# Optimization experiments

Hardware: AMD Instinct MI355X
Metric: run time of the kernel (lower is better)

Reference implementation:

```python
import jax, jax.numpy as jnp
import numpy as np

EPSILON = 0.1      # entropic regularization
N_ITERS = 50       # Sinkhorn fixed-point iterations
EPS_STAB = 1e-6    # numerical stabilizer (max(eps_stab, 1e-6) in original)
N, M, D = 8192, 8192, 128


def _sinkhorn_cost(X, Y):
    # squared Euclidean cost matrix (n, m)
    x2 = jnp.sum(X * X, axis=-1)
    y2 = jnp.sum(Y * Y, axis=-1)
    C = jnp.maximum(x2[:, None] + y2[None, :] - 2.0 * (X @ Y.T), 0.0)
    K = jnp.exp(-C / EPSILON)
    n, m = X.shape[0], Y.shape[0]
    a = jnp.full((n,), 1.0 / n, dtype=C.dtype)
    b = jnp.full((m,), 1.0 / m, dtype=C.dtype)

    def step(uv, _):
        u, v = uv
        Kv = K @ v + EPS_STAB
        u = jnp.where(jnp.abs(Kv) < EPS_STAB, a, a / jnp.maximum(Kv, EPS_STAB))
        Ktu = K.T @ u + EPS_STAB
        v = jnp.where(jnp.abs(Ktu) < EPS_STAB, b, b / jnp.maximum(Ktu, EPS_STAB))
        return (u, v), None

    (u, v), _ = jax.lax.scan(step, (jnp.ones_like(a), jnp.ones_like(b)), None, length=N_ITERS)
    # cost = sum(pi * C) with pi = u[:,None] * K * v[None,:], fused via einsum
    return jnp.einsum('i,ij,ij,j->', u, K, C, v)


def setup_inputs() -> dict:
    key = jax.random.key(0)
    k1, k2 = jax.random.split(key)
    # scale so squared distances ~O(1), commensurate with EPSILON
    X = jax.random.normal(k1, (N, D), dtype=jnp.float32) * 0.05
    Y = jax.random.normal(k2, (M, D), dtype=jnp.float32) * 0.05
    return {"X": X, "Y": Y}


def reference(X, Y):
    ot_xy = _sinkhorn_cost(X, Y)
    ot_xx = _sinkhorn_cost(X, jax.lax.stop_gradient(X))
    ot_yy = _sinkhorn_cost(Y, jax.lax.stop_gradient(Y))
    div = ot_xy - 0.5 * (ot_xx + ot_yy)
    div = jnp.where(jnp.isfinite(div), div, jnp.zeros_like(div))
    return jnp.maximum(div, 0.0)
```

## Files before the change

### kernel.cpp

```cpp
#include <hip/hip_runtime.h>

#define NPTS 8192
#define DIM  128
#define WPREP(x) (0.015625f / ((x) + 1.28e-4f))

typedef short s16x8 __attribute__((ext_vector_type(8)));
typedef float f32x4 __attribute__((ext_vector_type(4)));
typedef float f32x2 __attribute__((ext_vector_type(2)));

__device__ __forceinline__ ushort f2bf(float f) {
  unsigned u = __float_as_uint(f);
  u += 0x7fffu + ((u >> 16) & 1u);
  return (ushort)(u >> 16);
}
__device__ __forceinline__ float bf2f(ushort b) {
  return __uint_as_float(((unsigned)b) << 16);
}

__device__ __forceinline__ unsigned char fp8_enc_sw(float f) {
  if (f < 0.015625f) {
    int mi = (int)rintf(f * 512.0f);
    return (unsigned char)(mi >= 8 ? 0x08 : mi);
  }
  unsigned u = __float_as_uint(f);
  unsigned r = u + 0xfffffu + ((u >> 20) & 1u);
  int e = (int)((r >> 23) & 0xff) - 127;
  unsigned mant = (r >> 20) & 7u;
  if (e > 8 || (e == 8 && mant > 6)) return 0x7e;
  return (unsigned char)(((e + 7) << 3) | mant);
}
__device__ __forceinline__ float fp8_dec_sw(unsigned b) {
  unsigned E = (b >> 3) & 15u, M = b & 7u;
  float n = __uint_as_float(((E + 120u) << 23) | (M << 20));
  float s = (float)M * 0.001953125f;
  return E ? n : s;
}
__device__ __forceinline__ unsigned char enc1(float f) {
#if __has_builtin(__builtin_amdgcn_cvt_pk_fp8_f32)
  return (unsigned char)(__builtin_amdgcn_cvt_pk_fp8_f32(f, f, 0, false) & 0xff);
#else
  return fp8_enc_sw(f);
#endif
}
template <bool HI>
__device__ __forceinline__ f32x2 dec2(unsigned w) {
#if __has_builtin(__builtin_amdgcn_cvt_pk_f32_fp8)
  return __builtin_amdgcn_cvt_pk_f32_fp8((int)w, HI);
#else
  f32x2 r;
  r.x = fp8_dec_sw(HI ? ((w >> 16) & 0xffu) : (w & 0xffu));
  r.y = fp8_dec_sw(HI ? (w >> 24) : ((w >> 8) & 0xffu));
  return r;
#endif
}

__device__ __forceinline__ int swz(int j) { return j + 2 * (j >> 5); }
#define WSZ (NPTS + 2 * (NPTS / 32) + 8)

__global__ __launch_bounds__(256) void init_zero2(float* __restrict__ a,
                                                  float* __restrict__ b) {
  int j = blockIdx.x * 256 + threadIdx.x;
  a[j] = 0.0f; b[j] = 0.0f;
}

__global__ __launch_bounds__(256) void sq_rows(const float* __restrict__ X,
                                               const float* __restrict__ Y,
                                               float* __restrict__ x2,
                                               float* __restrict__ y2) {
  int wave = threadIdx.x >> 6, lane = threadIdx.x & 63;
  int row = blockIdx.x * 4 + wave;
  const float* src = (row < NPTS) ? X + (size_t)row * DIM
                                  : Y + (size_t)(row - NPTS) * DIM;
  float2 v = *reinterpret_cast<const float2*>(src + lane * 2);
  float ax = bf2f(f2bf(v.x)), ay = bf2f(f2bf(v.y));
  float s = ax * ax + ay * ay;
  for (int off = 32; off; off >>= 1) s += __shfl_down(s, off, 64);
  if (lane == 0) {
    if (row < NPTS) x2[row] = s; else y2[row - NPTS] = s;
  }
}

__global__ __launch_bounds__(256) void build_k(const float* __restrict__ A,
                                               const float* __restrict__ B,
                                               const float* __restrict__ a2,
                                               const float* __restrict__ b2,
                                               unsigned char* __restrict__ K8) {
  __shared__ ushort At[128][136];
  __shared__ ushort Bt[128][136];
  int t = threadIdx.x;
  int tm = blockIdx.x, tn = blockIdx.y;
  {
    int r = t >> 1;
    int c0 = (t & 1) * 64;
    const float* Ar = A + (size_t)(tm * 128 + r) * DIM + c0;
    const float* Br = B + (size_t)(tn * 128 + r) * DIM + c0;
    for (int c = 0; c < 64; c += 4) {
      float4 av = *reinterpret_cast<const float4*>(Ar + c);
      float4 bv = *reinterpret_cast<const float4*>(Br + c);
      unsigned pa0 = (unsigned)f2bf(av.x) | ((unsigned)f2bf(av.y) << 16);
      unsigned pa1 = (unsigned)f2bf(av.z) | ((unsigned)f2bf(av.w) << 16);
      unsigned pb0 = (unsigned)f2bf(bv.x) | ((unsigned)f2bf(bv.y) << 16);
      unsigned pb1 = (unsigned)f2bf(bv.z) | ((unsigned)f2bf(bv.w) << 16);
      *reinterpret_cast<unsigned*>(&At[r][c0 + c + 0]) = pa0;
      *reinterpret_cast<unsigned*>(&At[r][c0 + c + 2]) = pa1;
      *reinterpret_cast<unsigned*>(&Bt[r][c0 + c + 0]) = pb0;
      *reinterpret_cast<unsigned*>(&Bt[r][c0 + c + 2]) = pb1;
    }
  }
  __syncthreads();
  int wave = t >> 6, lane = t & 63;
  int lr = lane & 15;
  int lk = (lane >> 4) * 8;
  f32x4 acc[2][8];
  for (int mi = 0; mi < 2; ++mi)
    for (int ni = 0; ni < 8; ++ni)
      acc[mi][ni] = (f32x4){0.f, 0.f, 0.f, 0.f};
  for (int kc = 0; kc < 4; ++kc) {
    s16x8 af[2], bfr[8];
    af[0] = *reinterpret_cast<const s16x8*>(&At[wave * 32 + lr][kc * 32 + lk]);
    af[1] = *reinterpret_cast<const s16x8*>(&At[wave * 32 + 16 + lr][kc * 32 + lk]);
    for (int ni = 0; ni < 8; ++ni)
      bfr[ni] = *reinterpret_cast<const s16x8*>(&Bt[ni * 16 + lr][kc * 32 + lk]);
    for (int mi = 0; mi < 2; ++mi)
      for (int ni = 0; ni < 8; ++ni)
        acc[mi][ni] = __builtin_amdgcn_mfma_f32_16x16x32_bf16(af[mi], bfr[ni],
                                                              acc[mi][ni], 0, 0, 0);
  }
  int drow = (lane >> 4) * 4;
  float a2r[2][4], b2c[8];
  for (int mi = 0; mi < 2; ++mi)
    for (int r = 0; r < 4; ++r) a2r[mi][r] = a2[tm * 128 + wave * 32 + mi * 16 + drow + r];
  for (int ni = 0; ni < 8; ++ni) b2c[ni] = b2[tn * 128 + ni * 16 + lr];
  __syncthreads();
  unsigned char (*O)[144] = reinterpret_cast<unsigned char (*)[144]>(&At[0][0]);
  for (int mi = 0; mi < 2; ++mi)
    for (int ni = 0; ni < 8; ++ni)
      for (int r = 0; r < 4; ++r) {
        float S = acc[mi][ni][r];
        float C = fmaxf(a2r[mi][r] + b2c[ni] - 2.0f * S, 0.0f);
        float kv = exp2f(7.0f - 14.426950408889634f * C);
        O[wave * 32 + mi * 16 + drow + r][ni * 16 + lr] = enc1(kv);
      }
  __syncthreads();
  int row = t >> 1, half = t & 1;
  const uint4* src = reinterpret_cast<const uint4*>(&O[row][half * 64]);
  uint4* dst = reinterpret_cast<uint4*>(K8 + (size_t)(tm * 128 + row) * NPTS + tn * 128 + half * 64);
#pragma unroll
  for (int k = 0; k < 4; ++k) dst[k] = src[k];
}

__global__ __launch_bounds__(256) void sympass2(const unsigned char* __restrict__ KA,
                                                const unsigned char* __restrict__ KB,
                                                const float* __restrict__ inA,
                                                const float* __restrict__ inB,
                                                float* __restrict__ accA,
                                                float* __restrict__ accB,
                                                float* __restrict__ znA,
                                                float* __restrict__ znB,
                                                int init) {
  __shared__ unsigned char T[128][132];
  __shared__ float wj[128], wi[128];
  __shared__ float cp[8][128];
  int half = blockIdx.y;
  const unsigned char* K8 = half ? KB : KA;
  const float* in = half ? inB : inA;
  float* acc = half ? accB : accA;
  float* zn = half ? znB : znA;
  int tid = blockIdx.x;
  int t = threadIdx.x;
  if (tid < 32) zn[tid * 256 + t] = 0.0f;
  int bi = (int)(64.5f - sqrtf(64.5f * 64.5f - 2.0f * (float)tid));
  if (bi < 0) bi = 0; if (bi > 63) bi = 63;
  while (bi > 0 && tid < bi * 64 - bi * (bi - 1) / 2) --bi;
  while (tid >= (bi + 1) * 64 - (bi + 1) * bi / 2) ++bi;
  int bj = bi + tid - (bi * 64 - bi * (bi - 1) / 2);
  if (t < 128) wj[t] = init ? 1.0f : WPREP(in[bj * 128 + t]);
  else         wi[t - 128] = init ? 1.0f : WPREP(in[bi * 128 + (t - 128)]);
  int r = t >> 1, h = t & 1;
  const unsigned char* src = K8 + (size_t)(bi * 128 + r) * NPTS + bj * 128 + h * 64;
  uint4 q[4];
#pragma unroll
  for (int k = 0; k < 4; ++k) q[k] = *reinterpret_cast<const uint4*>(src + 16 * k);
  bool offdiag = (bi != bj);
  if (offdiag) {
#pragma unroll
    for (int k = 0; k < 4; ++k)
      *reinterpret_cast<uint4*>(&T[r][h * 64 + 16 * k]) = q[k];
  }
  __syncthreads();
  float racc = 0.f;
#pragma unroll
  for (int k = 0; k < 4; ++k) {
    const unsigned* p = &q[k].x;
#pragma unroll
    for (int e = 0; e < 4; ++e) {
      f32x2 lo = dec2<false>(p[e]), hi2 = dec2<true>(p[e]);
      int c = h * 64 + k * 16 + e * 4;
      racc = fmaf(lo.x, wj[c], racc);
      racc = fmaf(lo.y, wj[c + 1], racc);
      racc = fmaf(hi2.x, wj[c + 2], racc);
      racc = fmaf(hi2.y, wj[c + 3], racc);
    }
  }
  racc += __shfl_xor(racc, 1, 64);
  if (h == 0) atomicAdd(&acc[bi * 128 + r], racc);
  if (offdiag) {
    int cg = t >> 3, rg = t & 7;
    float c0 = 0.f, c1 = 0.f, c2 = 0.f, c3 = 0.f;
#pragma unroll
    for (int i = 0; i < 16; ++i) {
      int row = rg * 16 + ((i + rg * 2) & 15);
      unsigned v = *reinterpret_cast<const unsigned*>(&T[row][cg * 4]);
      float wr = wi[row];
      f32x2 lo = dec2<false>(v), hi2 = dec2<true>(v);
      c0 = fmaf(lo.x, wr, c0);
      c1 = fmaf(lo.y, wr, c1);
      c2 = fmaf(hi2.x, wr, c2);
      c3 = fmaf(hi2.y, wr, c3);
    }
    *reinterpret_cast<float4*>(&cp[rg][cg * 4]) = make_float4(c0, c1, c2, c3);
    __syncthreads();
    if (t < 128) {
      float s = (((cp[0][t] + cp[1][t]) + (cp[2][t] + cp[3][t])) +
                 ((cp[4][t] + cp[5][t]) + (cp[6][t] + cp[7][t])));
      atomicAdd(&acc[bj * 128 + t], s);
    }
  }
}

__device__ __forceinline__ void prep_w(float* w, const float* __restrict__ in, int init, int t) {
  if (init) {
#pragma unroll
    for (int k = 0; k < 16; ++k) w[swz(t + 512 * k)] = 1.0f;
  } else {
    float tmp[16];
#pragma unroll
    for (int k = 0; k < 16; ++k) tmp[k] = in[t + 512 * k];
#pragma unroll
    for (int k = 0; k < 16; ++k) w[swz(t + 512 * k)] = WPREP(tmp[k]);
  }
}

__device__ __forceinline__ void row_block(const unsigned char* __restrict__ K8,
                                          float* __restrict__ out,
                                          int row0, int t, const float* w) {
  int lane = t & 63;
  const unsigned char* K0 = K8 + (size_t)row0 * NPTS + lane * 16;
  const unsigned char* K1 = K0 + NPTS;
  float a0 = 0.f, b0 = 0.f, a1 = 0.f, b1 = 0.f;
  uint4 c0 = *reinterpret_cast<const uint4*>(K0);
  uint4 c1 = *reinterpret_cast<const uint4*>(K1);
#pragma unroll
  for (int rnd = 0; rnd < 8; ++rnd) {
    uint4 n0 = c0, n1 = c1;
    if (rnd < 7) {
      n0 = *reinterpret_cast<const uint4*>(K0 + (rnd + 1) * 1024);
      n1 = *reinterpret_cast<const uint4*>(K1 + (rnd + 1) * 1024);
    }
    int pb = swz(rnd * 1024 + lane * 16);
    const unsigned* p0 = &c0.x;
    const unsigned* p1 = &c1.x;
#pragma unroll
    for (int e = 0; e < 4; ++e) {
      f32x2 w0 = *reinterpret_cast<const f32x2*>(&w[pb + 4 * e]);
      f32x2 w1 = *reinterpret_cast<const f32x2*>(&w[pb + 4 * e + 2]);
      f32x2 k0l = dec2<false>(p0[e]), k0h = dec2<true>(p0[e]);
      f32x2 k1l = dec2<false>(p1[e]), k1h = dec2<true>(p1[e]);
      a0 = fmaf(k0l.x, w0.x, a0); b0 = fmaf(k0l.y, w0.y, b0);
      a0 = fmaf(k0h.x, w1.x, a0); b0 = fmaf(k0h.y, w1.y, b0);
      a1 = fmaf(k1l.x, w0.x, a1); b1 = fmaf(k1l.y, w0.y, b1);
      a1 = fmaf(k1h.x, w1.x, a1); b1 = fmaf(k1h.y, w1.y, b1);
    }
    c0 = n0; c1 = n1;
  }
  float s0 = a0 + b0, s1 = a1 + b1;
  for (int off = 32; off; off >>= 1) {
    s0 += __shfl_down(s0, off, 64);
    s1 += __shfl_down(s1, off, 64);
  }
  if (lane == 0) { out[row0] = s0; out[row0 + 1] = s1; }
}

__global__ __launch_bounds__(512) void rowpass_xy(const unsigned char* __restrict__ K8,
                                                  const float* __restrict__ in,
                                                  float* __restrict__ out,
                                                  float* __restrict__ vzero,
                                                  int init) {
  __shared__ float w[WSZ];
  int t = threadIdx.x;
  if (t < 16) vzero[blockIdx.x * 16 + t] = 0.0f;
  prep_w(w, in, init, t);
  __syncthreads();
  int row0 = blockIdx.x * 16 + (t >> 6) * 2;
  row_block(K8, out, row0, t, w);
}

__global__ __launch_bounds__(256) void colpass(const unsigned char* __restrict__ K8,
                                               const float* __restrict__ uraw,
                                               float* __restrict__ vout) {
  __shared__ float us[64];
  int t = threadIdx.x;
  int jb = blockIdx.x;
  int ic = blockIdx.y;
  int i0 = ic * 64;
  if (t < 64) us[t] = WPREP(uraw[i0 + t]);
  __syncthreads();
  int j0 = jb * 1024 + t * 4;
  float acc0 = 0.f, acc1 = 0.f, acc2 = 0.f, acc3 = 0.f;
  for (int i = 0; i < 64; i += 8) {
    unsigned wv[8];
#pragma unroll
    for (int k = 0; k < 8; ++k)
      wv[k] = *reinterpret_cast<const unsigned*>(K8 + (size_t)(i0 + i + k) * NPTS + j0);
#pragma unroll
    for (int k = 0; k < 8; ++k) {
      float uu = us[i + k];
      f32x2 lo = dec2<false>(wv[k]), hi = dec2<true>(wv[k]);
      acc0 = fmaf(lo.x, uu, acc0);
      acc1 = fmaf(lo.y, uu, acc1);
      acc2 = fmaf(hi.x, uu, acc2);
      acc3 = fmaf(hi.y, uu, acc3);
    }
  }
  atomicAdd(&vout[j0 + 0], acc0);
  atomicAdd(&vout[j0 + 1], acc1);
  atomicAdd(&vout[j0 + 2], acc2);
  atomicAdd(&vout[j0 + 3], acc3);
}

__global__ __launch_bounds__(256) void costpass(const unsigned char* __restrict__ K8,
                                                const float* __restrict__ uraw,
                                                const float* __restrict__ vraw,
                                                float* __restrict__ partial) {
  __shared__ float w[WSZ];
  __shared__ float wsum[4];
  int t = threadIdx.x;
  {
    float tmp[32];
#pragma unroll
    for (int k = 0; k < 32; ++k) tmp[k] = vraw[t + 256 * k];
#pragma unroll
    for (int k = 0; k < 32; ++k) w[swz(t + 256 * k)] = WPREP(tmp[k]);
  }
  __syncthreads();
  int wave = t >> 6, lane = t & 63;
  int row = blockIdx.x * 4 + wave;
  const unsigned char* Kr = K8 + (size_t)row * NPTS + lane * 16;
  float acc = 0.f;
  uint4 c = *reinterpret_cast<const uint4*>(Kr);
#pragma unroll
  for (int rnd = 0; rnd < 8; ++rnd) {
    uint4 n = c;
    if (rnd < 7) n = *reinterpret_cast<const uint4*>(Kr + (rnd + 1) * 1024);
    const unsigned* p = &c.x;
    int pb = swz(rnd * 1024 + lane * 16);
#pragma unroll
    for (int e = 0; e < 4; ++e) {
      f32x2 w0 = *reinterpret_cast<const f32x2*>(&w[pb + 4 * e]);
      f32x2 w1 = *reinterpret_cast<const f32x2*>(&w[pb + 4 * e + 2]);
      f32x2 kl = dec2<false>(p[e]), kh = dec2<true>(p[e]);
      float c0 = (kl.x > 0.f) ? 0.069314718f * (7.0f - __log2f(kl.x)) : 0.f;
      float c1 = (kl.y > 0.f) ? 0.069314718f * (7.0f - __log2f(kl.y)) : 0.f;
      float c2 = (kh.x > 0.f) ? 0.069314718f * (7.0f - __log2f(kh.x)) : 0.f;
      float c3 = (kh.y > 0.f) ? 0.069314718f * (7.0f - __log2f(kh.y)) : 0.f;
      acc = fmaf(kl.x * c0, w0.x, acc);
      acc = fmaf(kl.y * c1, w0.y, acc);
      acc = fmaf(kh.x * c2, w1.x, acc);
      acc = fmaf(kh.y * c3, w1.y, acc);
    }
    c = n;
  }
  for (int off = 32; off; off >>= 1) acc += __shfl_down(acc, off, 64);
  if (lane == 0) {
    float u = WPREP(uraw[row]);
    wsum[wave] = acc * u * 0.0078125f;
  }
  __syncthreads();
  if (t == 0) partial[blockIdx.x] = (wsum[0] + wsum[1]) + (wsum[2] + wsum[3]);
}

__global__ __launch_bounds__(256) void final_combine(const float* __restrict__ pxy,
                                                     const float* __restrict__ pxx,
                                                     const float* __restrict__ pyy,
                                                     float* __restrict__ out) {
  __shared__ float buf[3][256];
  int t = threadIdx.x;
  float s0 = 0.f, s1 = 0.f, s2 = 0.f;
  for (int i = t; i < 2048; i += 256) { s0 += pxy[i]; s1 += pxx[i]; s2 += pyy[i]; }
  buf[0][t] = s0; buf[1][t] = s1; buf[2][t] = s2;
  __syncthreads();
  for (int off = 128; off; off >>= 1) {
    if (t < off) {
      buf[0][t] += buf[0][t + off];
      buf[1][t] += buf[1][t + off];
      buf[2][t] += buf[2][t + off];
    }
    __syncthreads();
  }
  if (t == 0) {
    float div = buf[0][0] - 0.5f * (buf[1][0] + buf[2][0]);
    if (!isfinite(div)) div = 0.0f;
    out[0] = fmaxf(div, 0.0f);
  }
}

extern "C" void kernel_launch(void* const* d_in, const int* in_sizes, int n_in,
                              void* d_out, int out_size, void* d_ws, size_t ws_size,
                              hipStream_t stream) {
  const float* X = (const float*)d_in[0];
  const float* Y = (const float*)d_in[1];
  float* out = (float*)d_out;
  char* ws = (char*)d_ws;

  size_t off = 0;
  unsigned char* KA = (unsigned char*)(ws + off); off += (size_t)NPTS * NPTS;
  unsigned char* KB = (unsigned char*)(ws + off); off += (size_t)NPTS * NPTS;
  float* zA[3]; float* zB[3];
  for (int i = 0; i < 3; ++i) { zA[i] = (float*)(ws + off); off += (size_t)NPTS * 4; }
  for (int i = 0; i < 3; ++i) { zB[i] = (float*)(ws + off); off += (size_t)NPTS * 4; }
  float* rxy  = (float*)(ws + off); off += (size_t)NPTS * 4;
  float* vab0 = (float*)(ws + off); off += (size_t)NPTS * 4;
  float* vab1 = (float*)(ws + off); off += (size_t)NPTS * 4;
  float* x2   = (float*)(ws + off); off += (size_t)NPTS * 4;
  float* y2   = (float*)(ws + off); off += (size_t)NPTS * 4;
  float* pxy  = (float*)(ws + off); off += 2048 * 4;
  float* pxx  = (float*)(ws + off); off += 2048 * 4;
  float* pyy  = (float*)(ws + off); off += 2048 * 4;
  if (ws_size < off) {
    (void)hipMemsetAsync(d_out, 0, sizeof(float), stream);
    return;
  }
  float* vab[2] = {vab0, vab1};

  init_zero2<<<32, 256, 0, stream>>>(zA[1], zB[1]);
  sq_rows<<<4096, 256, 0, stream>>>(X, Y, x2, y2);

  build_k<<<dim3(64, 64), 256, 0, stream>>>(X, X, x2, x2, KA);
  build_k<<<dim3(64, 64), 256, 0, stream>>>(Y, Y, y2, y2, KB);
  for (int p = 1; p <= 100; ++p) {
    sympass2<<<dim3(2080, 2), 256, 0, stream>>>(KA, KB,
                                                zA[(p - 1) % 3], zB[(p - 1) % 3],
                                                zA[p % 3], zB[p % 3],
                                                zA[(p + 1) % 3], zB[(p + 1) % 3],
                                                p == 1 ? 1 : 0);
  }
  costpass<<<2048, 256, 0, stream>>>(KA, zA[0], zA[1], pxx);
  costpass<<<2048, 256, 0, stream>>>(KB, zB[0], zB[1], pyy);

  build_k<<<dim3(64, 64), 256, 0, stream>>>(X, Y, x2, y2, KA);
  for (int it = 0; it < 50; ++it) {
    rowpass_xy<<<512, 512, 0, stream>>>(KA, vab[it & 1], rxy,
                                        vab[(it + 1) & 1], it == 0 ? 1 : 0);
    colpass<<<dim3(8, 128), 256, 0, stream>>>(KA, rxy, vab[(it + 1) & 1]);
  }
  costpass<<<2048, 256, 0, stream>>>(KA, rxy, vab[0], pxy);

  final_combine<<<1, 256, 0, stream>>>(pxy, pxx, pyy, out);
}
```

Measured before the change: 3.994 ms.

## Fuse symmetric and cross Sinkhorn passes into one interleaved megakernel launch

```diff
diff --git a/kernel.cpp b/kernel.cpp
--- a/kernel.cpp
+++ b/kernel.cpp
@@ -149,6 +149,195 @@
   for (int k = 0; k < 4; ++k) dst[k] = src[k];
 }
 
+struct SymMem {
+  unsigned char T[128][132];
+  float wj[128], wi[128];
+  float cp[8][128];
+};
+
+__device__ __forceinline__ void sym_tile(const unsigned char* __restrict__ K8,
+                                         const float* __restrict__ in,
+                                         float* __restrict__ acc,
+                                         float* __restrict__ zn,
+                                         int tid, int init, SymMem& sm) {
+  int t = threadIdx.x;
+  if (tid < 32) zn[tid * 256 + t] = 0.0f;
+  int bi = (int)(64.5f - sqrtf(64.5f * 64.5f - 2.0f * (float)tid));
+  if (bi < 0) bi = 0; if (bi > 63) bi = 63;
+  while (bi > 0 && tid < bi * 64 - bi * (bi - 1) / 2) --bi;
+  while (tid >= (bi + 1) * 64 - (bi + 1) * bi / 2) ++bi;
+  int bj = bi + tid - (bi * 64 - bi * (bi - 1) / 2);
+  if (t < 128) sm.wj[t] = init ? 1.0f : WPREP(in[bj * 128 + t]);
+  else         sm.wi[t - 128] = init ? 1.0f : WPREP(in[bi * 128 + (t - 128)]);
+  int r = t >> 1, h = t & 1;
+  const unsigned char* src = K8 + (size_t)(bi * 128 + r) * NPTS + bj * 128 + h * 64;
+  uint4 q[4];
+#pragma unroll
+  for (int k = 0; k < 4; ++k) q[k] = *reinterpret_cast<const uint4*>(src + 16 * k);
+  bool offdiag = (bi != bj);
+  if (offdiag) {
+#pragma unroll
+    for (int k = 0; k < 4; ++k)
+      *reinterpret_cast<uint4*>(&sm.T[r][h * 64 + 16 * k]) = q[k];
+  }
+  __syncthreads();
+  float racc = 0.f;
+#pragma unroll
+  for (int k = 0; k < 4; ++k) {
+    const unsigned* p = &q[k].x;
+#pragma unroll
+    for (int e = 0; e < 4; ++e) {
+      f32x2 lo = dec2<false>(p[e]), hi2 = dec2<true>(p[e]);
+      int c = h * 64 + k * 16 + e * 4;
+      racc = fmaf(lo.x, sm.wj[c], racc);
+      racc = fmaf(lo.y, sm.wj[c + 1], racc);
+      racc = fmaf(hi2.x, sm.wj[c + 2], racc);
+      racc = fmaf(hi2.y, sm.wj[c + 3], racc);
+    }
+  }
+  racc += __shfl_xor(racc, 1, 64);
+  if (h == 0) atomicAdd(&acc[bi * 128 + r], racc);
+  if (offdiag) {
+    int cg = t >> 3, rg = t & 7;
+    float c0 = 0.f, c1 = 0.f, c2 = 0.f, c3 = 0.f;
+#pragma unroll
+    for (int i = 0; i < 16; ++i) {
+      int row = rg * 16 + ((i + rg * 2) & 15);
+      unsigned v = *reinterpret_cast<const unsigned*>(&sm.T[row][cg * 4]);
+      float wr = sm.wi[row];
+      f32x2 lo = dec2<false>(v), hi2 = dec2<true>(v);
+      c0 = fmaf(lo.x, wr, c0);
+      c1 = fmaf(lo.y, wr, c1);
+      c2 = fmaf(hi2.x, wr, c2);
+      c3 = fmaf(hi2.y, wr, c3);
+    }
+    *reinterpret_cast<float4*>(&sm.cp[rg][cg * 4]) = make_float4(c0, c1, c2, c3);
+    __syncthreads();
+    if (t < 128) {
+      float s = (((sm.cp[0][t] + sm.cp[1][t]) + (sm.cp[2][t] + sm.cp[3][t])) +
+                 ((sm.cp[4][t] + sm.cp[5][t]) + (sm.cp[6][t] + sm.cp[7][t])));
+      atomicAdd(&acc[bj * 128 + t], s);
+    }
+  }
+}
+
+__device__ __forceinline__ void row_block(const unsigned char* __restrict__ K8,
+                                          float* __restrict__ out,
+                                          int row0, int t, const float* w) {
+  int lane = t & 63;
+  const unsigned char* K0 = K8 + (size_t)row0 * NPTS + lane * 16;
+  const unsigned char* K1 = K0 + NPTS;
+  float a0 = 0.f, b0 = 0.f, a1 = 0.f, b1 = 0.f;
+  uint4 c0 = *reinterpret_cast<const uint4*>(K0);
+  uint4 c1 = *reinterpret_cast<const uint4*>(K1);
+#pragma unroll
+  for (int rnd = 0; rnd < 8; ++rnd) {
+    uint4 n0 = c0, n1 = c1;
+    if (rnd < 7) {
+      n0 = *reinterpret_cast<const uint4*>(K0 + (rnd + 1) * 1024);
+      n1 = *reinterpret_cast<const uint4*>(K1 + (rnd + 1) * 1024);
+    }
+    int pb = swz(rnd * 1024 + lane * 16);
+    const unsigned* p0 = &c0.x;
+    const unsigned* p1 = &c1.x;
+#pragma unroll
+    for (int e = 0; e < 4; ++e) {
+      f32x2 w0 = *reinterpret_cast<const f32x2*>(&w[pb + 4 * e]);
+      f32x2 w1 = *reinterpret_cast<const f32x2*>(&w[pb + 4 * e + 2]);
+      f32x2 k0l = dec2<false>(p0[e]), k0h = dec2<true>(p0[e]);
+      f32x2 k1l = dec2<false>(p1[e]), k1h = dec2<true>(p1[e]);
+      a0 = fmaf(k0l.x, w0.x, a0); b0 = fmaf(k0l.y, w0.y, b0);
+      a0 = fmaf(k0h.x, w1.x, a0); b0 = fmaf(k0h.y, w1.y, b0);
+      a1 = fmaf(k1l.x, w0.x, a1); b1 = fmaf(k1l.y, w0.y, b1);
+      a1 = fmaf(k1h.x, w1.x, a1); b1 = fmaf(k1h.y, w1.y, b1);
+    }
+    c0 = n0; c1 = n1;
+  }
+  float s0 = a0 + b0, s1 = a1 + b1;
+  for (int off = 32; off; off >>= 1) {
+    s0 += __shfl_down(s0, off, 64);
+    s1 += __shfl_down(s1, off, 64);
+  }
+  if (lane == 0) { out[row0] = s0; out[row0 + 1] = s1; }
+}
+
+union MegaMem {
+  SymMem sym;
+  float w[WSZ];
+  float us[64];
+};
+
+__global__ __launch_bounds__(256) void megapass(const unsigned char* __restrict__ KA,
+                                                const unsigned char* __restrict__ KB,
+                                                const unsigned char* __restrict__ KXY,
+                                                const float* __restrict__ inA,
+                                                const float* __restrict__ inB,
+                                                float* __restrict__ accA,
+                                                float* __restrict__ accB,
+                                                float* __restrict__ znA,
+                                                float* __restrict__ znB,
+                                                const float* __restrict__ xyin,
+                                                float* __restrict__ rxy,
+                                                float* __restrict__ vabn,
+                                                int p, int xyrole) {
+  __shared__ MegaMem sm;
+  int bx = blockIdx.x;
+  int t = threadIdx.x;
+  bool isxy = (bx % 5 == 4) && (bx < 5120);
+  if (isxy) {
+    int xyi = bx / 5;
+    if (xyrole == 0) {
+      if (t < 8) vabn[xyi * 8 + t] = 0.0f;
+      if (p == 1) {
+#pragma unroll
+        for (int k = 0; k < 32; ++k) sm.w[swz(t + 256 * k)] = 1.0f;
+      } else {
+        float tmp[32];
+#pragma unroll
+        for (int k = 0; k < 32; ++k) tmp[k] = xyin[t + 256 * k];
+#pragma unroll
+        for (int k = 0; k < 32; ++k) sm.w[swz(t + 256 * k)] = WPREP(tmp[k]);
+      }
+      __syncthreads();
+      int row0 = xyi * 8 + (t >> 6) * 2;
+      row_block(KXY, rxy, row0, t, sm.w);
+    } else {
+      int jb = xyi & 7, ic = xyi >> 3;
+      int i0 = ic * 64;
+      if (t < 64) sm.us[t] = WPREP(rxy[i0 + t]);
+      __syncthreads();
+      int j0 = jb * 1024 + t * 4;
+      float acc0 = 0.f, acc1 = 0.f, acc2 = 0.f, acc3 = 0.f;
+      for (int i = 0; i < 64; i += 8) {
+        unsigned wv[8];
+#pragma unroll
+        for (int k = 0; k < 8; ++k)
+          wv[k] = *reinterpret_cast<const unsigned*>(KXY + (size_t)(i0 + i + k) * NPTS + j0);
+#pragma unroll
+        for (int k = 0; k < 8; ++k) {
+          float uu = sm.us[i + k];
+          f32x2 lo = dec2<false>(wv[k]), hi = dec2<true>(wv[k]);
+          acc0 = fmaf(lo.x, uu, acc0);
+          acc1 = fmaf(lo.y, uu, acc1);
+          acc2 = fmaf(hi.x, uu, acc2);
+          acc3 = fmaf(hi.y, uu, acc3);
+        }
+      }
+      atomicAdd(&vabn[j0 + 0], acc0);
+      atomicAdd(&vabn[j0 + 1], acc1);
+      atomicAdd(&vabn[j0 + 2], acc2);
+      atomicAdd(&vabn[j0 + 3], acc3);
+    }
+  } else {
+    int nxy_below = (bx < 5120) ? ((bx + 1) / 5) : 1024;
+    int symi = bx - nxy_below;
+    int half = symi & 1;
+    int tid = symi >> 1;
+    sym_tile(half ? KB : KA, half ? inB : inA, half ? accB : accA,
+             half ? znB : znA, tid, p == 1 ? 1 : 0, sm.sym);
+  }
+}
+
 __global__ __launch_bounds__(256) void sympass2(const unsigned char* __restrict__ KA,
                                                 const unsigned char* __restrict__ KB,
                                                 const float* __restrict__ inA,
@@ -158,77 +347,13 @@
                                                 float* __restrict__ znA,
                                                 float* __restrict__ znB,
                                                 int init) {
-  __shared__ unsigned char T[128][132];
-  __shared__ float wj[128], wi[128];
-  __shared__ float cp[8][128];
+  __shared__ SymMem sm;
   int half = blockIdx.y;
-  const unsigned char* K8 = half ? KB : KA;
-  const float* in = half ? inB : inA;
-  float* acc = half ? accB : accA;
-  float* zn = half ? znB : znA;
-  int tid = blockIdx.x;
-  int t = threadIdx.x;
-  if (tid < 32) zn[tid * 256 + t] = 0.0f;
-  int bi = (int)(64.5f - sqrtf(64.5f * 64.5f - 2.0f * (float)tid));
-  if (bi < 0) bi = 0; if (bi > 63) bi = 63;
-  while (bi > 0 && tid < bi * 64 - bi * (bi - 1) / 2) --bi;
-  while (tid >= (bi + 1) * 64 - (bi + 1) * bi / 2) ++bi;
-  int bj = bi + tid - (bi * 64 - bi * (bi - 1) / 2);
-  if (t < 128) wj[t] = init ? 1.0f : WPREP(in[bj * 128 + t]);
-  else         wi[t - 128] = init ? 1.0f : WPREP(in[bi * 128 + (t - 128)]);
-  int r = t >> 1, h = t & 1;
-  const unsigned char* src = K8 + (size_t)(bi * 128 + r) * NPTS + bj * 128 + h * 64;
-  uint4 q[4];
-#pragma unroll
-  for (int k = 0; k < 4; ++k) q[k] = *reinterpret_cast<const uint4*>(src + 16 * k);
-  bool offdiag = (bi != bj);
-  if (offdiag) {
-#pragma unroll
-    for (int k = 0; k < 4; ++k)
-      *reinterpret_cast<uint4*>(&T[r][h * 64 + 16 * k]) = q[k];
-  }
-  __syncthreads();
-  float racc = 0.f;
-#pragma unroll
-  for (int k = 0; k < 4; ++k) {
-    const unsigned* p = &q[k].x;
-#pragma unroll
-    for (int e = 0; e < 4; ++e) {
-      f32x2 lo = dec2<false>(p[e]), hi2 = dec2<true>(p[e]);
-      int c = h * 64 + k * 16 + e * 4;
-      racc = fmaf(lo.x, wj[c], racc);
-      racc = fmaf(lo.y, wj[c + 1], racc);
-      racc = fmaf(hi2.x, wj[c + 2], racc);
-      racc = fmaf(hi2.y, wj[c + 3], racc);
-    }
-  }
-  racc += __shfl_xor(racc, 1, 64);
-  if (h == 0) atomicAdd(&acc[bi * 128 + r], racc);
-  if (offdiag) {
-    int cg = t >> 3, rg = t & 7;
-    float c0 = 0.f, c1 = 0.f, c2 = 0.f, c3 = 0.f;
-#pragma unroll
-    for (int i = 0; i < 16; ++i) {
-      int row = rg * 16 + ((i + rg * 2) & 15);
-      unsigned v = *reinterpret_cast<const unsigned*>(&T[row][cg * 4]);
-      float wr = wi[row];
-      f32x2 lo = dec2<false>(v), hi2 = dec2<true>(v);
-      c0 = fmaf(lo.x, wr, c0);
-      c1 = fmaf(lo.y, wr, c1);
-      c2 = fmaf(hi2.x, wr, c2);
-      c3 = fmaf(hi2.y, wr, c3);
-    }
-    *reinterpret_cast<float4*>(&cp[rg][cg * 4]) = make_float4(c0, c1, c2, c3);
-    __syncthreads();
-    if (t < 128) {
-      float s = (((cp[0][t] + cp[1][t]) + (cp[2][t] + cp[3][t])) +
-                 ((cp[4][t] + cp[5][t]) + (cp[6][t] + cp[7][t])));
-      atomicAdd(&acc[bj * 128 + t], s);
-    }
-  }
-}
-
-__device__ __forceinline__ void prep_w(float* w, const float* __restrict__ in, int init, int t) {
+  sym_tile(half ? KB : KA, half ? inB : inA, half ? accB : accA,
+           half ? znB : znA, blockIdx.x, init, sm);
+}
+
+__device__ __forceinline__ void prep_w512(float* w, const float* __restrict__ in, int init, int t) {
   if (init) {
 #pragma unroll
     for (int k = 0; k < 16; ++k) w[swz(t + 512 * k)] = 1.0f;
@@ -239,46 +364,6 @@
 #pragma unroll
     for (int k = 0; k < 16; ++k) w[swz(t + 512 * k)] = WPREP(tmp[k]);
   }
-}
-
-__device__ __forceinline__ void row_block(const unsigned char* __restrict__ K8,
-                                          float* __restrict__ out,
-                                          int row0, int t, const float* w) {
-  int lane = t & 63;
-  const unsigned char* K0 = K8 + (size_t)row0 * NPTS + lane * 16;
-  const unsigned char* K1 = K0 + NPTS;
-  float a0 = 0.f, b0 = 0.f, a1 = 0.f, b1 = 0.f;
-  uint4 c0 = *reinterpret_cast<const uint4*>(K0);
-  uint4 c1 = *reinterpret_cast<const uint4*>(K1);
-#pragma unroll
-  for (int rnd = 0; rnd < 8; ++rnd) {
-    uint4 n0 = c0, n1 = c1;
-    if (rnd < 7) {
-      n0 = *reinterpret_cast<const uint4*>(K0 + (rnd + 1) * 1024);
-      n1 = *reinterpret_cast<const uint4*>(K1 + (rnd + 1) * 1024);
-    }
-    int pb = swz(rnd * 1024 + lane * 16);
-    const unsigned* p0 = &c0.x;
-    const unsigned* p1 = &c1.x;
-#pragma unroll
-    for (int e = 0; e < 4; ++e) {
-      f32x2 w0 = *reinterpret_cast<const f32x2*>(&w[pb + 4 * e]);
-      f32x2 w1 = *reinterpret_cast<const f32x2*>(&w[pb + 4 * e + 2]);
-      f32x2 k0l = dec2<false>(p0[e]), k0h = dec2<true>(p0[e]);
-      f32x2 k1l = dec2<false>(p1[e]), k1h = dec2<true>(p1[e]);
-      a0 = fmaf(k0l.x, w0.x, a0); b0 = fmaf(k0l.y, w0.y, b0);
-      a0 = fmaf(k0h.x, w1.x, a0); b0 = fmaf(k0h.y, w1.y, b0);
-      a1 = fmaf(k1l.x, w0.x, a1); b1 = fmaf(k1l.y, w0.y, b1);
-      a1 = fmaf(k1h.x, w1.x, a1); b1 = fmaf(k1h.y, w1.y, b1);
-    }
-    c0 = n0; c1 = n1;
-  }
-  float s0 = a0 + b0, s1 = a1 + b1;
-  for (int off = 32; off; off >>= 1) {
-    s0 += __shfl_down(s0, off, 64);
-    s1 += __shfl_down(s1, off, 64);
-  }
-  if (lane == 0) { out[row0] = s0; out[row0 + 1] = s1; }
 }
 
 __global__ __launch_bounds__(512) void rowpass_xy(const unsigned char* __restrict__ K8,
@@ -289,7 +374,7 @@
   __shared__ float w[WSZ];
   int t = threadIdx.x;
   if (t < 16) vzero[blockIdx.x * 16 + t] = 0.0f;
-  prep_w(w, in, init, t);
+  prep_w512(w, in, init, t);
   __syncthreads();
   int row0 = blockIdx.x * 16 + (t >> 6) * 2;
   row_block(K8, out, row0, t, w);
@@ -426,7 +511,10 @@
   float* pxy  = (float*)(ws + off); off += 2048 * 4;
   float* pxx  = (float*)(ws + off); off += 2048 * 4;
   float* pyy  = (float*)(ws + off); off += 2048 * 4;
-  if (ws_size < off) {
+  size_t need_base = off;
+  unsigned char* KXY = (unsigned char*)(ws + off); off += (size_t)NPTS * NPTS;
+  bool fused = (ws_size >= off);
+  if (ws_size < need_base) {
     (void)hipMemsetAsync(d_out, 0, sizeof(float), stream);
     return;
   }
@@ -435,25 +523,44 @@
   init_zero2<<<32, 256, 0, stream>>>(zA[1], zB[1]);
   sq_rows<<<4096, 256, 0, stream>>>(X, Y, x2, y2);
 
-  build_k<<<dim3(64, 64), 256, 0, stream>>>(X, X, x2, x2, KA);
-  build_k<<<dim3(64, 64), 256, 0, stream>>>(Y, Y, y2, y2, KB);
-  for (int p = 1; p <= 100; ++p) {
-    sympass2<<<dim3(2080, 2), 256, 0, stream>>>(KA, KB,
-                                                zA[(p - 1) % 3], zB[(p - 1) % 3],
-                                                zA[p % 3], zB[p % 3],
-                                                zA[(p + 1) % 3], zB[(p + 1) % 3],
-                                                p == 1 ? 1 : 0);
-  }
-  costpass<<<2048, 256, 0, stream>>>(KA, zA[0], zA[1], pxx);
-  costpass<<<2048, 256, 0, stream>>>(KB, zB[0], zB[1], pyy);
-
-  build_k<<<dim3(64, 64), 256, 0, stream>>>(X, Y, x2, y2, KA);
-  for (int it = 0; it < 50; ++it) {
-    rowpass_xy<<<512, 512, 0, stream>>>(KA, vab[it & 1], rxy,
-                                        vab[(it + 1) & 1], it == 0 ? 1 : 0);
-    colpass<<<dim3(8, 128), 256, 0, stream>>>(KA, rxy, vab[(it + 1) & 1]);
-  }
-  costpass<<<2048, 256, 0, stream>>>(KA, rxy, vab[0], pxy);
+  if (fused) {
+    build_k<<<dim3(64, 64), 256, 0, stream>>>(X, X, x2, x2, KA);
+    build_k<<<dim3(64, 64), 256, 0, stream>>>(Y, Y, y2, y2, KB);
+    build_k<<<dim3(64, 64), 256, 0, stream>>>(X, Y, x2, y2, KXY);
+    for (int k = 0; k < 100; ++k) {
+      int p = k + 1;
+      int it = k >> 1;
+      int role = k & 1;
+      megapass<<<5184, 256, 0, stream>>>(KA, KB, KXY,
+                                         zA[(p - 1) % 3], zB[(p - 1) % 3],
+                                         zA[p % 3], zB[p % 3],
+                                         zA[(p + 1) % 3], zB[(p + 1) % 3],
+                                         vab[it & 1], rxy, vab[(it + 1) & 1],
+                                         p, role);
+    }
+    costpass<<<2048, 256, 0, stream>>>(KA, zA[0], zA[1], pxx);
+    costpass<<<2048, 256, 0, stream>>>(KB, zB[0], zB[1], pyy);
+    costpass<<<2048, 256, 0, stream>>>(KXY, rxy, vab[0], pxy);
+  } else {
+    build_k<<<dim3(64, 64), 256, 0, stream>>>(X, X, x2, x2, KA);
+    build_k<<<dim3(64, 64), 256, 0, stream>>>(Y, Y, y2, y2, KB);
+    for (int p = 1; p <= 100; ++p) {
+      sympass2<<<dim3(2080, 2), 256, 0, stream>>>(KA, KB,
+                                                  zA[(p - 1) % 3], zB[(p - 1) % 3],
+                                                  zA[p % 3], zB[p % 3],
+                                                  zA[(p + 1) % 3], zB[(p + 1) % 3],
+                                                  p == 1 ? 1 : 0);
+    }
+    costpass<<<2048, 256, 0, stream>>>(KA, zA[0], zA[1], pxx);
+    costpass<<<2048, 256, 0, stream>>>(KB, zB[0], zB[1], pyy);
+    build_k<<<dim3(64, 64), 256, 0, stream>>>(X, Y, x2, y2, KA);
+    for (int it = 0; it < 50; ++it) {
+      rowpass_xy<<<512, 512, 0, stream>>>(KA, vab[it & 1], rxy,
+                                          vab[(it + 1) & 1], it == 0 ? 1 : 0);
+      colpass<<<dim3(8, 128), 256, 0, stream>>>(KA, rxy, vab[(it + 1) & 1]);
+    }
+    costpass<<<2048, 256, 0, stream>>>(KA, rxy, vab[0], pxy);
+  }
 
   final_combine<<<1, 256, 0, stream>>>(pxy, pxx, pyy, out);
 }
```

Result: faster. 3.312 ms (-17.1%).
